# Performance work log

Hardware: AMD Instinct MI355X
Metric: run time of the kernel (lower is better)

Reference implementation:

```python
import jax, jax.numpy as jnp
import numpy as np

N = 50000      # nodes
E = 800000     # edges
D_IN = 300     # input node feature dim
D_H = 96       # hidden dim
D_OUT = 2      # classes
G = 64         # graphs in batch


def setup_inputs() -> dict:
    key = jax.random.key(0)
    ks = jax.random.split(key, 10)
    x = jax.random.normal(ks[0], (N, D_IN), dtype=jnp.float32)
    src = jax.random.randint(ks[1], (E,), 0, N, dtype=jnp.int32)
    dst = jax.random.randint(ks[2], (E,), 0, N, dtype=jnp.int32)
    batch = jnp.sort(jax.random.randint(ks[3], (N,), 0, G, dtype=jnp.int32))
    # GCNConv: linear weight (no bias in lin), separate additive bias (PyG default)
    W1 = jax.random.normal(ks[4], (D_IN, D_H), jnp.float32) / np.sqrt(D_IN)
    b1 = jnp.zeros((D_H,), jnp.float32)
    W2 = jax.random.normal(ks[5], (D_H, D_H), jnp.float32) / np.sqrt(D_H)
    b2 = jnp.zeros((D_H,), jnp.float32)
    Wfc = jax.random.normal(ks[6], (D_H, D_OUT), jnp.float32) / np.sqrt(D_H)
    bfc = jnp.zeros((D_OUT,), jnp.float32)
    return {"x": x, "W1": W1, "b1": b1, "W2": W2, "b2": b2,
            "Wfc": Wfc, "bfc": bfc, "src": src, "dst": dst, "batch": batch}


def _gcn_conv(h_in, W, b, src, dst, deg_inv_sqrt):
    """PyG GCNConv with self-loops: out = D^-1/2 (A+I) D^-1/2 (h W) + b."""
    h = h_in @ W                                   # [N, F] transform first
    norm = deg_inv_sqrt[src] * deg_inv_sqrt[dst]   # [E]
    msg = h[src] * norm[:, None]                   # gather + scale (dominant traffic)
    agg = jax.ops.segment_sum(msg, dst, num_segments=N)
    agg = agg + h * (deg_inv_sqrt * deg_inv_sqrt)[:, None]  # self-loop term
    return agg + b


def reference(x, W1, b1, W2, b2, Wfc, bfc, src, dst, batch):
    # degree with self loops, computed on destination nodes (PyG convention)
    deg = jax.ops.segment_sum(jnp.ones((E,), x.dtype), dst, num_segments=N) + 1.0
    dis = jax.lax.rsqrt(deg)
    h = jax.nn.relu(_gcn_conv(x, W1, b1, src, dst, dis))   # dropout = identity (eval)
    h = jax.nn.relu(_gcn_conv(h, W2, b2, src, dst, dis))
    # global mean pool over per-graph node segments
    counts = jax.ops.segment_sum(jnp.ones((N,), x.dtype), batch, num_segments=G)
    pooled = jax.ops.segment_sum(h, batch, num_segments=G) / jnp.maximum(counts, 1.0)[:, None]
    return pooled @ Wfc + bfc                               # [G, D_OUT]
```

## Files before the change

kernel.cpp:

```cpp
#include <hip/hip_runtime.h>
#include <hip/hip_bf16.h>

#define NN 50000
#define NE 800000
#define DIN 300
#define KP1 320
#define DH 96
#define DOUTC 2
#define NG 64

#define NKB 10
#define NFRAG (NKB * 6 * 64)

#define DSTRIDE 64
#define NB1 ((NN + 63) / 64)
#define EPB 1024
#define NB2 ((NN + 31) / 32)
#define LROW 104
#define QW 12

typedef __attribute__((ext_vector_type(8))) short bf16x8;
typedef __attribute__((ext_vector_type(4))) float f32x4;

__device__ inline unsigned short f2bf(float f) {
    unsigned int u = __float_as_uint(f);
    unsigned int r = (u + 0x7fffu + ((u >> 16) & 1u)) >> 16;
    return (unsigned short)r;
}
__device__ inline float b2f(unsigned short u) {
    return __uint_as_float((unsigned int)u << 16);
}
__device__ inline float blo(unsigned int u) { return __uint_as_float(u << 16); }
__device__ inline float bhi(unsigned int u) { return __uint_as_float(u & 0xffff0000u); }

__global__ void k_prep(int* cnt, float* pooled,
                       const float* __restrict__ W1, unsigned short* __restrict__ wt1f,
                       const float* __restrict__ W2, unsigned short* __restrict__ wt2) {
    int i = blockIdx.x * blockDim.x + threadIdx.x;
    if (i < NN) cnt[i] = 0;
    if (i < NG * DH) pooled[i] = 0.f;
    if (i < NFRAG * 8) {
        int j = i & 7;
        int f = i >> 3;
        int lane = f & 63;
        int ft = f >> 6;
        int t = ft % 6;
        int kb = ft / 6;
        int row = (lane & 15) + 16 * t;
        int col = kb * 32 + (lane >> 4) * 8 + j;
        wt1f[i] = (col < DIN) ? f2bf(W1[(size_t)col * DH + row]) : (unsigned short)0;
    }
    if (i < DH * DH) {
        int j = i / DH, k = i - j * DH;
        wt2[i] = f2bf(W2[(size_t)k * DH + j]);
    }
}

__global__ __launch_bounds__(256) void k_g1sc(const float* __restrict__ A,
        const unsigned short* __restrict__ WF, unsigned short* __restrict__ Cb,
        const int* __restrict__ src, const int* __restrict__ dst,
        int* cnt, unsigned short* __restrict__ esrc) {
    __shared__ unsigned short ldsB[NFRAG * 8];
    const int tid = threadIdx.x;

    if (blockIdx.x & 1) {
        const int ebase = (blockIdx.x >> 1) * EPB + tid * 4;
        if (ebase + 3 < NE) {
            int4 d4 = *(const int4*)&dst[ebase];
            int4 s4 = *(const int4*)&src[ebase];
            int p0 = atomicAdd(&cnt[d4.x], 1);
            int p1 = atomicAdd(&cnt[d4.y], 1);
            int p2 = atomicAdd(&cnt[d4.z], 1);
            int p3 = atomicAdd(&cnt[d4.w], 1);
            if (p0 < DSTRIDE) esrc[(size_t)d4.x * DSTRIDE + p0] = (unsigned short)s4.x;
            if (p1 < DSTRIDE) esrc[(size_t)d4.y * DSTRIDE + p1] = (unsigned short)s4.y;
            if (p2 < DSTRIDE) esrc[(size_t)d4.z * DSTRIDE + p2] = (unsigned short)s4.z;
            if (p3 < DSTRIDE) esrc[(size_t)d4.w * DSTRIDE + p3] = (unsigned short)s4.w;
        } else {
            for (int e = ebase; e < NE; ++e) {
                int d = dst[e];
                int pos = atomicAdd(&cnt[d], 1);
                if (pos < DSTRIDE) esrc[(size_t)d * DSTRIDE + pos] = (unsigned short)src[e];
            }
        }
        return;
    }

    const int tile = blockIdx.x >> 1;
    {
        const uint4* srcv = (const uint4*)WF;
        uint4* dstv = (uint4*)ldsB;
        #pragma unroll
        for (int f = 0; f < NFRAG / 256; ++f)
            dstv[f * 256 + tid] = srcv[f * 256 + tid];
    }
    __syncthreads();

    const int wv = tid >> 6;
    const int lane = tid & 63;
    const int m = lane & 15;
    const int quad = lane >> 4;
    const int row = tile * 64 + wv * 16 + m;
    const int arow = row < NN ? row : NN - 1;
    const float* ap = A + (size_t)arow * DIN + quad * 8;
    const float4 z4 = make_float4(0.f, 0.f, 0.f, 0.f);
    const bf16x8* lb = (const bf16x8*)ldsB;
    f32x4 acc[6];
    #pragma unroll
    for (int t = 0; t < 6; ++t) acc[t] = (f32x4){0.f, 0.f, 0.f, 0.f};

    float4 pa[4][2];
    #pragma unroll
    for (int i = 0; i < 3; ++i) {
        int kb = i * 32 + quad * 8;
        pa[i][0] = (kb + 4 <= DIN) ? *(const float4*)(ap + i * 32) : z4;
        pa[i][1] = (kb + 8 <= DIN) ? *(const float4*)(ap + i * 32 + 4) : z4;
    }

    #pragma unroll
    for (int i = 0; i < NKB; ++i) {
        if (i + 3 < NKB) {
            int kb = (i + 3) * 32 + quad * 8;
            pa[(i + 3) & 3][0] = (kb + 4 <= DIN) ? *(const float4*)(ap + (i + 3) * 32) : z4;
            pa[(i + 3) & 3][1] = (kb + 8 <= DIN) ? *(const float4*)(ap + (i + 3) * 32 + 4) : z4;
        }
        float4 a0 = pa[i & 3][0], a1 = pa[i & 3][1];
        bf16x8 af;
        af[0] = (short)f2bf(a0.x); af[1] = (short)f2bf(a0.y);
        af[2] = (short)f2bf(a0.z); af[3] = (short)f2bf(a0.w);
        af[4] = (short)f2bf(a1.x); af[5] = (short)f2bf(a1.y);
        af[6] = (short)f2bf(a1.z); af[7] = (short)f2bf(a1.w);
        #pragma unroll
        for (int t = 0; t < 6; ++t) {
            bf16x8 bf = lb[(i * 6 + t) * 64 + lane];
            acc[t] = __builtin_amdgcn_mfma_f32_16x16x32_bf16(af, bf, acc[t], 0, 0, 0);
        }
    }
    const int rbase = tile * 64 + wv * 16 + quad * 4;
    #pragma unroll
    for (int r = 0; r < 4; ++r) {
        int rr = rbase + r;
        if (rr < NN) {
            unsigned short* cp = Cb + (size_t)rr * DH + m;
            #pragma unroll
            for (int t = 0; t < 6; ++t) cp[t * 16] = f2bf(acc[t][r]);
        }
    }
}

__device__ inline void agg_row8(const uint4* __restrict__ hbq, const int* __restrict__ cnt,
                                const unsigned short* __restrict__ esrc,
                                int n, int q, float dn, int count, float* acc) {
    uint4 u0 = hbq[(size_t)n * QW + q];
    acc[0] = dn * blo(u0.x); acc[1] = dn * bhi(u0.x);
    acc[2] = dn * blo(u0.y); acc[3] = dn * bhi(u0.y);
    acc[4] = dn * blo(u0.z); acc[5] = dn * bhi(u0.z);
    acc[6] = dn * blo(u0.w); acc[7] = dn * bhi(u0.w);
    const int beg = n * DSTRIDE;
    const int end = beg + count;
    int e = beg;
    for (; e + 7 < end; e += 8) {
        int s0 = esrc[e],     s1 = esrc[e + 1], s2 = esrc[e + 2], s3 = esrc[e + 3];
        int s4 = esrc[e + 4], s5 = esrc[e + 5], s6 = esrc[e + 6], s7 = esrc[e + 7];
        uint4 v0 = hbq[(size_t)s0 * QW + q];
        uint4 v1 = hbq[(size_t)s1 * QW + q];
        uint4 v2 = hbq[(size_t)s2 * QW + q];
        uint4 v3 = hbq[(size_t)s3 * QW + q];
        uint4 v4 = hbq[(size_t)s4 * QW + q];
        uint4 v5 = hbq[(size_t)s5 * QW + q];
        uint4 v6 = hbq[(size_t)s6 * QW + q];
        uint4 v7 = hbq[(size_t)s7 * QW + q];
        float d0 = rsqrtf(1.0f + (float)cnt[s0]);
        float d1 = rsqrtf(1.0f + (float)cnt[s1]);
        float d2 = rsqrtf(1.0f + (float)cnt[s2]);
        float d3 = rsqrtf(1.0f + (float)cnt[s3]);
        float d4 = rsqrtf(1.0f + (float)cnt[s4]);
        float d5 = rsqrtf(1.0f + (float)cnt[s5]);
        float d6 = rsqrtf(1.0f + (float)cnt[s6]);
        float d7 = rsqrtf(1.0f + (float)cnt[s7]);
        acc[0] = fmaf(d0, blo(v0.x), acc[0]); acc[1] = fmaf(d0, bhi(v0.x), acc[1]);
        acc[2] = fmaf(d0, blo(v0.y), acc[2]); acc[3] = fmaf(d0, bhi(v0.y), acc[3]);
        acc[4] = fmaf(d0, blo(v0.z), acc[4]); acc[5] = fmaf(d0, bhi(v0.z), acc[5]);
        acc[6] = fmaf(d0, blo(v0.w), acc[6]); acc[7] = fmaf(d0, bhi(v0.w), acc[7]);
        acc[0] = fmaf(d1, blo(v1.x), acc[0]); acc[1] = fmaf(d1, bhi(v1.x), acc[1]);
        acc[2] = fmaf(d1, blo(v1.y), acc[2]); acc[3] = fmaf(d1, bhi(v1.y), acc[3]);
        acc[4] = fmaf(d1, blo(v1.z), acc[4]); acc[5] = fmaf(d1, bhi(v1.z), acc[5]);
        acc[6] = fmaf(d1, blo(v1.w), acc[6]); acc[7] = fmaf(d1, bhi(v1.w), acc[7]);
        acc[0] = fmaf(d2, blo(v2.x), acc[0]); acc[1] = fmaf(d2, bhi(v2.x), acc[1]);
        acc[2] = fmaf(d2, blo(v2.y), acc[2]); acc[3] = fmaf(d2, bhi(v2.y), acc[3]);
        acc[4] = fmaf(d2, blo(v2.z), acc[4]); acc[5] = fmaf(d2, bhi(v2.z), acc[5]);
        acc[6] = fmaf(d2, blo(v2.w), acc[6]); acc[7] = fmaf(d2, bhi(v2.w), acc[7]);
        acc[0] = fmaf(d3, blo(v3.x), acc[0]); acc[1] = fmaf(d3, bhi(v3.x), acc[1]);
        acc[2] = fmaf(d3, blo(v3.y), acc[2]); acc[3] = fmaf(d3, bhi(v3.y), acc[3]);
        acc[4] = fmaf(d3, blo(v3.z), acc[4]); acc[5] = fmaf(d3, bhi(v3.z), acc[5]);
        acc[6] = fmaf(d3, blo(v3.w), acc[6]); acc[7] = fmaf(d3, bhi(v3.w), acc[7]);
        acc[0] = fmaf(d4, blo(v4.x), acc[0]); acc[1] = fmaf(d4, bhi(v4.x), acc[1]);
        acc[2] = fmaf(d4, blo(v4.y), acc[2]); acc[3] = fmaf(d4, bhi(v4.y), acc[3]);
        acc[4] = fmaf(d4, blo(v4.z), acc[4]); acc[5] = fmaf(d4, bhi(v4.z), acc[5]);
        acc[6] = fmaf(d4, blo(v4.w), acc[6]); acc[7] = fmaf(d4, bhi(v4.w), acc[7]);
        acc[0] = fmaf(d5, blo(v5.x), acc[0]); acc[1] = fmaf(d5, bhi(v5.x), acc[1]);
        acc[2] = fmaf(d5, blo(v5.y), acc[2]); acc[3] = fmaf(d5, bhi(v5.y), acc[3]);
        acc[4] = fmaf(d5, blo(v5.z), acc[4]); acc[5] = fmaf(d5, bhi(v5.z), acc[5]);
        acc[6] = fmaf(d5, blo(v5.w), acc[6]); acc[7] = fmaf(d5, bhi(v5.w), acc[7]);
        acc[0] = fmaf(d6, blo(v6.x), acc[0]); acc[1] = fmaf(d6, bhi(v6.x), acc[1]);
        acc[2] = fmaf(d6, blo(v6.y), acc[2]); acc[3] = fmaf(d6, bhi(v6.y), acc[3]);
        acc[4] = fmaf(d6, blo(v6.z), acc[4]); acc[5] = fmaf(d6, bhi(v6.z), acc[5]);
        acc[6] = fmaf(d6, blo(v6.w), acc[6]); acc[7] = fmaf(d6, bhi(v6.w), acc[7]);
        acc[0] = fmaf(d7, blo(v7.x), acc[0]); acc[1] = fmaf(d7, bhi(v7.x), acc[1]);
        acc[2] = fmaf(d7, blo(v7.y), acc[2]); acc[3] = fmaf(d7, bhi(v7.y), acc[3]);
        acc[4] = fmaf(d7, blo(v7.z), acc[4]); acc[5] = fmaf(d7, bhi(v7.z), acc[5]);
        acc[6] = fmaf(d7, blo(v7.w), acc[6]); acc[7] = fmaf(d7, bhi(v7.w), acc[7]);
    }
    for (; e + 3 < end; e += 4) {
        int s0 = esrc[e], s1 = esrc[e + 1], s2 = esrc[e + 2], s3 = esrc[e + 3];
        float d0 = rsqrtf(1.0f + (float)cnt[s0]);
        float d1 = rsqrtf(1.0f + (float)cnt[s1]);
        float d2 = rsqrtf(1.0f + (float)cnt[s2]);
        float d3 = rsqrtf(1.0f + (float)cnt[s3]);
        uint4 v0 = hbq[(size_t)s0 * QW + q];
        uint4 v1 = hbq[(size_t)s1 * QW + q];
        uint4 v2 = hbq[(size_t)s2 * QW + q];
        uint4 v3 = hbq[(size_t)s3 * QW + q];
        acc[0] = fmaf(d0, blo(v0.x), acc[0]); acc[1] = fmaf(d0, bhi(v0.x), acc[1]);
        acc[2] = fmaf(d0, blo(v0.y), acc[2]); acc[3] = fmaf(d0, bhi(v0.y), acc[3]);
        acc[4] = fmaf(d0, blo(v0.z), acc[4]); acc[5] = fmaf(d0, bhi(v0.z), acc[5]);
        acc[6] = fmaf(d0, blo(v0.w), acc[6]); acc[7] = fmaf(d0, bhi(v0.w), acc[7]);
        acc[0] = fmaf(d1, blo(v1.x), acc[0]); acc[1] = fmaf(d1, bhi(v1.x), acc[1]);
        acc[2] = fmaf(d1, blo(v1.y), acc[2]); acc[3] = fmaf(d1, bhi(v1.y), acc[3]);
        acc[4] = fmaf(d1, blo(v1.z), acc[4]); acc[5] = fmaf(d1, bhi(v1.z), acc[5]);
        acc[6] = fmaf(d1, blo(v1.w), acc[6]); acc[7] = fmaf(d1, bhi(v1.w), acc[7]);
        acc[0] = fmaf(d2, blo(v2.x), acc[0]); acc[1] = fmaf(d2, bhi(v2.x), acc[1]);
        acc[2] = fmaf(d2, blo(v2.y), acc[2]); acc[3] = fmaf(d2, bhi(v2.y), acc[3]);
        acc[4] = fmaf(d2, blo(v2.z), acc[4]); acc[5] = fmaf(d2, bhi(v2.z), acc[5]);
        acc[6] = fmaf(d2, blo(v2.w), acc[6]); acc[7] = fmaf(d2, bhi(v2.w), acc[7]);
        acc[0] = fmaf(d3, blo(v3.x), acc[0]); acc[1] = fmaf(d3, bhi(v3.x), acc[1]);
        acc[2] = fmaf(d3, blo(v3.y), acc[2]); acc[3] = fmaf(d3, bhi(v3.y), acc[3]);
        acc[4] = fmaf(d3, blo(v3.z), acc[4]); acc[5] = fmaf(d3, bhi(v3.z), acc[5]);
        acc[6] = fmaf(d3, blo(v3.w), acc[6]); acc[7] = fmaf(d3, bhi(v3.w), acc[7]);
    }
    for (; e < end; ++e) {
        int s = esrc[e];
        float ds = rsqrtf(1.0f + (float)cnt[s]);
        uint4 v = hbq[(size_t)s * QW + q];
        acc[0] = fmaf(ds, blo(v.x), acc[0]); acc[1] = fmaf(ds, bhi(v.x), acc[1]);
        acc[2] = fmaf(ds, blo(v.y), acc[2]); acc[3] = fmaf(ds, bhi(v.y), acc[3]);
        acc[4] = fmaf(ds, blo(v.z), acc[4]); acc[5] = fmaf(ds, bhi(v.z), acc[5]);
        acc[6] = fmaf(ds, blo(v.w), acc[6]); acc[7] = fmaf(ds, bhi(v.w), acc[7]);
    }
}

__global__ __launch_bounds__(384) void k_agg1g2(const uint4* __restrict__ hbq,
        const int* __restrict__ cnt, const unsigned short* __restrict__ esrc,
        const float* __restrict__ b1, const unsigned short* __restrict__ WT,
        unsigned short* __restrict__ Cb) {
    __shared__ unsigned short a1l[32 * LROW];
    const int tid = threadIdx.x;
    const int n0 = blockIdx.x * 32;

    {
        int nl = tid / QW;
        int q = tid - nl * QW;
        int n = n0 + nl;
        uint4 o = make_uint4(0, 0, 0, 0);
        if (n < NN) {
            int count = cnt[n];
            float dn = rsqrtf(1.0f + (float)count);
            if (count > DSTRIDE) count = DSTRIDE;
            float acc[8];
            agg_row8(hbq, cnt, esrc, n, q, dn, count, acc);
            float r[8];
            #pragma unroll
            for (int k = 0; k < 8; ++k)
                r[k] = fmaxf(fmaf(dn, acc[k], b1[q * 8 + k]), 0.f);
            o.x = (unsigned int)f2bf(r[0]) | ((unsigned int)f2bf(r[1]) << 16);
            o.y = (unsigned int)f2bf(r[2]) | ((unsigned int)f2bf(r[3]) << 16);
            o.z = (unsigned int)f2bf(r[4]) | ((unsigned int)f2bf(r[5]) << 16);
            o.w = (unsigned int)f2bf(r[6]) | ((unsigned int)f2bf(r[7]) << 16);
        }
        *(uint4*)&a1l[nl * LROW + q * 8] = o;
    }
    __syncthreads();

    if (tid < 128) {
        const int wv = tid >> 6;
        const int lane = tid & 63;
        const int m = lane & 15;
        const int quad = lane >> 4;
        const unsigned short* ap = &a1l[(wv * 16 + m) * LROW + quad * 8];
        const unsigned short* wp = WT + (size_t)m * DH + quad * 8;
        bf16x8 af[3];
        #pragma unroll
        for (int i = 0; i < 3; ++i) af[i] = *(const bf16x8*)(ap + i * 32);
        const int rbase = n0 + wv * 16 + quad * 4;
        #pragma unroll 1
        for (int t = 0; t < 6; ++t) {
            f32x4 acc = (f32x4){0.f, 0.f, 0.f, 0.f};
            #pragma unroll
            for (int i = 0; i < 3; ++i) {
                bf16x8 bf = *(const bf16x8*)(wp + (size_t)t * 16 * DH + i * 32);
                acc = __builtin_amdgcn_mfma_f32_16x16x32_bf16(af[i], bf, acc, 0, 0, 0);
            }
            #pragma unroll
            for (int r = 0; r < 4; ++r) {
                int rr = rbase + r;
                if (rr < NN) Cb[(size_t)rr * DH + m + t * 16] = f2bf(acc[r]);
            }
        }
    }
}

__global__ __launch_bounds__(256) void k_agg2pool(const uint4* __restrict__ hbq,
        const int* __restrict__ cnt, const unsigned short* __restrict__ esrc,
        const float* __restrict__ b2, const int* __restrict__ batch,
        float* __restrict__ pooled) {
    __shared__ float lpool[4 * DH];
    __shared__ int g0s;
    const int tid = threadIdx.x;
    for (int i = tid; i < 4 * DH; i += 256) lpool[i] = 0.f;
    if (tid == 0) {
        int nfirst = (blockIdx.x * 256) / QW;
        g0s = batch[nfirst < NN ? nfirst : NN - 1];
    }
    __syncthreads();
    const int g0 = g0s;
    const int gid = blockIdx.x * 256 + tid;
    if (gid < NN * QW) {
        int n = gid / QW;
        int q = gid - n * QW;
        int count = cnt[n];
        float dn = rsqrtf(1.0f + (float)count);
        if (count > DSTRIDE) count = DSTRIDE;
        float acc[8];
        agg_row8(hbq, cnt, esrc, n, q, dn, count, acc);
        float r[8];
        #pragma unroll
        for (int k = 0; k < 8; ++k)
            r[k] = fmaxf(fmaf(dn, acc[k], b2[q * 8 + k]), 0.f);
        int g = batch[n];
        int slot = g - g0;
        if (slot < 4) {
            float* lp = &lpool[slot * DH + q * 8];
            #pragma unroll
            for (int k = 0; k < 8; ++k) atomicAdd(&lp[k], r[k]);
        } else {
            float* gp = &pooled[(size_t)g * DH + q * 8];
            #pragma unroll
            for (int k = 0; k < 8; ++k) atomicAdd(&gp[k], r[k]);
        }
    }
    __syncthreads();
    for (int i = tid; i < 4 * DH; i += 256) {
        float v = lpool[i];
        if (v != 0.f) {
            int slot = i / DH, f = i - slot * DH;
            atomicAdd(&pooled[(size_t)(g0 + slot) * DH + f], v);
        }
    }
}

__global__ void k_fc(const float* __restrict__ pooled, const int* __restrict__ batch,
                     const float* __restrict__ Wfc, const float* __restrict__ bfc,
                     float* __restrict__ out) {
    const int t = threadIdx.x;
    if (t >= NG * DOUTC) return;
    const int g = t / DOUTC;
    const int c = t - g * DOUTC;
    int lo = 0, hi = NN;
    while (lo < hi) { int mid = (lo + hi) >> 1; if (batch[mid] < g) lo = mid + 1; else hi = mid; }
    const int s = lo;
    hi = NN;
    while (lo < hi) { int mid = (lo + hi) >> 1; if (batch[mid] < g + 1) lo = mid + 1; else hi = mid; }
    float inv = 1.f / fmaxf((float)(lo - s), 1.f);
    float acc = bfc[c];
    #pragma unroll 8
    for (int j = 0; j < DH; ++j)
        acc += pooled[g * DH + j] * inv * Wfc[j * DOUTC + c];
    out[g * DOUTC + c] = acc;
}

extern "C" void kernel_launch(void* const* d_in, const int* in_sizes, int n_in,
                              void* d_out, int out_size, void* d_ws, size_t ws_size,
                              hipStream_t stream) {
    const float* x   = (const float*)d_in[0];
    const float* W1  = (const float*)d_in[1];
    const float* b1  = (const float*)d_in[2];
    const float* W2  = (const float*)d_in[3];
    const float* b2  = (const float*)d_in[4];
    const float* Wfc = (const float*)d_in[5];
    const float* bfc = (const float*)d_in[6];
    const int* src   = (const int*)d_in[7];
    const int* dst   = (const int*)d_in[8];
    const int* batch = (const int*)d_in[9];
    float* out = (float*)d_out;

    unsigned short* hb  = (unsigned short*)d_ws;
    unsigned short* h2b = hb + (size_t)NN * DH;
    float* pooled= (float*)(h2b + (size_t)NN * DH);
    int* cnt     = (int*)(pooled + NG * DH);
    unsigned short* esrc = (unsigned short*)(cnt + NN);
    unsigned short* wt1f = esrc + (size_t)NN * DSTRIDE;
    unsigned short* wt2  = wt1f + NFRAG * 8;

    const int TB = 256;
    k_prep<<<(NN + TB - 1) / TB, TB, 0, stream>>>(cnt, pooled, W1, wt1f, W2, wt2);
    k_g1sc<<<NB1 * 2, 256, 0, stream>>>(x, wt1f, hb, src, dst, cnt, esrc);
    k_agg1g2<<<NB2, 384, 0, stream>>>((const uint4*)hb, cnt, esrc, b1, wt2, h2b);
    k_agg2pool<<<(NN * QW + TB - 1) / TB, TB, 0, stream>>>(
        (const uint4*)h2b, cnt, esrc, b2, batch, pooled);
    k_fc<<<1, 128, 0, stream>>>(pooled, batch, Wfc, bfc, out);
}
```

Before: 250.7 us.

## Split each node's edge list across two thread halves in aggregation kernels

Both aggregation kernels now process 16 nodes per 384-thread block, and two threads share each (node, feature-quad) pair. Each thread gathers half of the node's edges, and the two partial sums are combined through shared memory. This doubles gather parallelism and memory-level parallelism per node, so each thread's serial edge chain is shorter and the long random-gather latency is better hidden. In exchange it adds an extra __syncthreads and shared-memory round trip, and the MFMA stage now uses only one wave per block.

```diff
diff --git a/kernel.cpp b/kernel.cpp
--- a/kernel.cpp
+++ b/kernel.cpp
@@ -15,7 +15,8 @@
 #define DSTRIDE 64
 #define NB1 ((NN + 63) / 64)
 #define EPB 1024
-#define NB2 ((NN + 31) / 32)
+#define NPB 16
+#define NBA ((NN + NPB - 1) / NPB)
 #define LROW 104
 #define QW 12
 
@@ -26,9 +27,6 @@
     unsigned int u = __float_as_uint(f);
     unsigned int r = (u + 0x7fffu + ((u >> 16) & 1u)) >> 16;
     return (unsigned short)r;
-}
-__device__ inline float b2f(unsigned short u) {
-    return __uint_as_float((unsigned int)u << 16);
 }
 __device__ inline float blo(unsigned int u) { return __uint_as_float(u << 16); }
 __device__ inline float bhi(unsigned int u) { return __uint_as_float(u & 0xffff0000u); }
@@ -148,17 +146,9 @@
     }
 }
 
-__device__ inline void agg_row8(const uint4* __restrict__ hbq, const int* __restrict__ cnt,
-                                const unsigned short* __restrict__ esrc,
-                                int n, int q, float dn, int count, float* acc) {
-    uint4 u0 = hbq[(size_t)n * QW + q];
-    acc[0] = dn * blo(u0.x); acc[1] = dn * bhi(u0.x);
-    acc[2] = dn * blo(u0.y); acc[3] = dn * bhi(u0.y);
-    acc[4] = dn * blo(u0.z); acc[5] = dn * bhi(u0.z);
-    acc[6] = dn * blo(u0.w); acc[7] = dn * bhi(u0.w);
-    const int beg = n * DSTRIDE;
-    const int end = beg + count;
-    int e = beg;
+__device__ inline void agg_edges(const uint4* __restrict__ hbq, const int* __restrict__ cnt,
+                                 const unsigned short* __restrict__ esrc,
+                                 int q, int e, int end, float* acc) {
     for (; e + 7 < end; e += 8) {
         int s0 = esrc[e],     s1 = esrc[e + 1], s2 = esrc[e + 2], s3 = esrc[e + 3];
         int s4 = esrc[e + 4], s5 = esrc[e + 5], s6 = esrc[e + 6], s7 = esrc[e + 7];
@@ -253,103 +243,156 @@
         const int* __restrict__ cnt, const unsigned short* __restrict__ esrc,
         const float* __restrict__ b1, const unsigned short* __restrict__ WT,
         unsigned short* __restrict__ Cb) {
-    __shared__ unsigned short a1l[32 * LROW];
+    __shared__ unsigned short a1l[NPB * LROW];
+    __shared__ float hacc[NPB * QW][8];
     const int tid = threadIdx.x;
-    const int n0 = blockIdx.x * 32;
-
-    {
-        int nl = tid / QW;
-        int q = tid - nl * QW;
-        int n = n0 + nl;
+    const int n0 = blockIdx.x * NPB;
+    const int h = tid / (NPB * QW);
+    const int r = tid - h * (NPB * QW);
+    const int nl = r / QW;
+    const int q = r - nl * QW;
+    const int n = n0 + nl;
+
+    int count = 0, beg = 0, c0 = 0;
+    float dn = 1.f;
+    if (n < NN) {
+        count = cnt[n];
+        dn = rsqrtf(1.0f + (float)count);
+        if (count > DSTRIDE) count = DSTRIDE;
+        beg = n * DSTRIDE;
+        c0 = count >> 1;
+    }
+    float acc[8] = {0.f, 0.f, 0.f, 0.f, 0.f, 0.f, 0.f, 0.f};
+    if (n < NN) {
+        if (h == 0) {
+            uint4 u0 = hbq[(size_t)n * QW + q];
+            acc[0] = dn * blo(u0.x); acc[1] = dn * bhi(u0.x);
+            acc[2] = dn * blo(u0.y); acc[3] = dn * bhi(u0.y);
+            acc[4] = dn * blo(u0.z); acc[5] = dn * bhi(u0.z);
+            acc[6] = dn * blo(u0.w); acc[7] = dn * bhi(u0.w);
+            agg_edges(hbq, cnt, esrc, q, beg, beg + c0, acc);
+        } else {
+            agg_edges(hbq, cnt, esrc, q, beg + c0, beg + count, acc);
+        }
+    }
+    if (h == 1) {
+        #pragma unroll
+        for (int k = 0; k < 8; ++k) hacc[r][k] = acc[k];
+    }
+    __syncthreads();
+    if (h == 0) {
         uint4 o = make_uint4(0, 0, 0, 0);
         if (n < NN) {
-            int count = cnt[n];
-            float dn = rsqrtf(1.0f + (float)count);
-            if (count > DSTRIDE) count = DSTRIDE;
-            float acc[8];
-            agg_row8(hbq, cnt, esrc, n, q, dn, count, acc);
-            float r[8];
+            const float* hp = hacc[r];
+            float rr[8];
             #pragma unroll
             for (int k = 0; k < 8; ++k)
-                r[k] = fmaxf(fmaf(dn, acc[k], b1[q * 8 + k]), 0.f);
-            o.x = (unsigned int)f2bf(r[0]) | ((unsigned int)f2bf(r[1]) << 16);
-            o.y = (unsigned int)f2bf(r[2]) | ((unsigned int)f2bf(r[3]) << 16);
-            o.z = (unsigned int)f2bf(r[4]) | ((unsigned int)f2bf(r[5]) << 16);
-            o.w = (unsigned int)f2bf(r[6]) | ((unsigned int)f2bf(r[7]) << 16);
+                rr[k] = fmaxf(fmaf(dn, acc[k] + hp[k], b1[q * 8 + k]), 0.f);
+            o.x = (unsigned int)f2bf(rr[0]) | ((unsigned int)f2bf(rr[1]) << 16);
+            o.y = (unsigned int)f2bf(rr[2]) | ((unsigned int)f2bf(rr[3]) << 16);
+            o.z = (unsigned int)f2bf(rr[4]) | ((unsigned int)f2bf(rr[5]) << 16);
+            o.w = (unsigned int)f2bf(rr[6]) | ((unsigned int)f2bf(rr[7]) << 16);
         }
         *(uint4*)&a1l[nl * LROW + q * 8] = o;
     }
     __syncthreads();
 
-    if (tid < 128) {
-        const int wv = tid >> 6;
-        const int lane = tid & 63;
+    if (tid < 64) {
+        const int lane = tid;
         const int m = lane & 15;
         const int quad = lane >> 4;
-        const unsigned short* ap = &a1l[(wv * 16 + m) * LROW + quad * 8];
+        const unsigned short* ap = &a1l[m * LROW + quad * 8];
         const unsigned short* wp = WT + (size_t)m * DH + quad * 8;
         bf16x8 af[3];
         #pragma unroll
         for (int i = 0; i < 3; ++i) af[i] = *(const bf16x8*)(ap + i * 32);
-        const int rbase = n0 + wv * 16 + quad * 4;
+        const int rbase = n0 + quad * 4;
         #pragma unroll 1
         for (int t = 0; t < 6; ++t) {
-            f32x4 acc = (f32x4){0.f, 0.f, 0.f, 0.f};
+            f32x4 acc2 = (f32x4){0.f, 0.f, 0.f, 0.f};
             #pragma unroll
             for (int i = 0; i < 3; ++i) {
                 bf16x8 bf = *(const bf16x8*)(wp + (size_t)t * 16 * DH + i * 32);
-                acc = __builtin_amdgcn_mfma_f32_16x16x32_bf16(af[i], bf, acc, 0, 0, 0);
+                acc2 = __builtin_amdgcn_mfma_f32_16x16x32_bf16(af[i], bf, acc2, 0, 0, 0);
             }
             #pragma unroll
-            for (int r = 0; r < 4; ++r) {
-                int rr = rbase + r;
-                if (rr < NN) Cb[(size_t)rr * DH + m + t * 16] = f2bf(acc[r]);
+            for (int rr2 = 0; rr2 < 4; ++rr2) {
+                int row = rbase + rr2;
+                if (row < NN) Cb[(size_t)row * DH + m + t * 16] = f2bf(acc2[rr2]);
             }
         }
     }
 }
 
-__global__ __launch_bounds__(256) void k_agg2pool(const uint4* __restrict__ hbq,
+__global__ __launch_bounds__(384) void k_agg2pool(const uint4* __restrict__ hbq,
         const int* __restrict__ cnt, const unsigned short* __restrict__ esrc,
         const float* __restrict__ b2, const int* __restrict__ batch,
         float* __restrict__ pooled) {
     __shared__ float lpool[4 * DH];
+    __shared__ float hacc[NPB * QW][8];
     __shared__ int g0s;
     const int tid = threadIdx.x;
-    for (int i = tid; i < 4 * DH; i += 256) lpool[i] = 0.f;
+    for (int i = tid; i < 4 * DH; i += 384) lpool[i] = 0.f;
     if (tid == 0) {
-        int nfirst = (blockIdx.x * 256) / QW;
-        g0s = batch[nfirst < NN ? nfirst : NN - 1];
+        int nf = blockIdx.x * NPB;
+        g0s = batch[nf < NN ? nf : NN - 1];
     }
     __syncthreads();
     const int g0 = g0s;
-    const int gid = blockIdx.x * 256 + tid;
-    if (gid < NN * QW) {
-        int n = gid / QW;
-        int q = gid - n * QW;
-        int count = cnt[n];
-        float dn = rsqrtf(1.0f + (float)count);
+    const int n0 = blockIdx.x * NPB;
+    const int h = tid / (NPB * QW);
+    const int r = tid - h * (NPB * QW);
+    const int nl = r / QW;
+    const int q = r - nl * QW;
+    const int n = n0 + nl;
+
+    int count = 0, beg = 0, c0 = 0;
+    float dn = 1.f;
+    if (n < NN) {
+        count = cnt[n];
+        dn = rsqrtf(1.0f + (float)count);
         if (count > DSTRIDE) count = DSTRIDE;
-        float acc[8];
-        agg_row8(hbq, cnt, esrc, n, q, dn, count, acc);
-        float r[8];
+        beg = n * DSTRIDE;
+        c0 = count >> 1;
+    }
+    float acc[8] = {0.f, 0.f, 0.f, 0.f, 0.f, 0.f, 0.f, 0.f};
+    if (n < NN) {
+        if (h == 0) {
+            uint4 u0 = hbq[(size_t)n * QW + q];
+            acc[0] = dn * blo(u0.x); acc[1] = dn * bhi(u0.x);
+            acc[2] = dn * blo(u0.y); acc[3] = dn * bhi(u0.y);
+            acc[4] = dn * blo(u0.z); acc[5] = dn * bhi(u0.z);
+            acc[6] = dn * blo(u0.w); acc[7] = dn * bhi(u0.w);
+            agg_edges(hbq, cnt, esrc, q, beg, beg + c0, acc);
+        } else {
+            agg_edges(hbq, cnt, esrc, q, beg + c0, beg + count, acc);
+        }
+    }
+    if (h == 1) {
+        #pragma unroll
+        for (int k = 0; k < 8; ++k) hacc[r][k] = acc[k];
+    }
+    __syncthreads();
+    if (h == 0 && n < NN) {
+        const float* hp = hacc[r];
+        float rr[8];
         #pragma unroll
         for (int k = 0; k < 8; ++k)
-            r[k] = fmaxf(fmaf(dn, acc[k], b2[q * 8 + k]), 0.f);
+            rr[k] = fmaxf(fmaf(dn, acc[k] + hp[k], b2[q * 8 + k]), 0.f);
         int g = batch[n];
         int slot = g - g0;
         if (slot < 4) {
             float* lp = &lpool[slot * DH + q * 8];
             #pragma unroll
-            for (int k = 0; k < 8; ++k) atomicAdd(&lp[k], r[k]);
+            for (int k = 0; k < 8; ++k) atomicAdd(&lp[k], rr[k]);
         } else {
             float* gp = &pooled[(size_t)g * DH + q * 8];
             #pragma unroll
-            for (int k = 0; k < 8; ++k) atomicAdd(&gp[k], r[k]);
-        }
-    }
-    __syncthreads();
-    for (int i = tid; i < 4 * DH; i += 256) {
+            for (int k = 0; k < 8; ++k) atomicAdd(&gp[k], rr[k]);
+        }
+    }
+    __syncthreads();
+    for (int i = tid; i < 4 * DH; i += 384) {
         float v = lpool[i];
         if (v != 0.f) {
             int slot = i / DH, f = i - slot * DH;
@@ -404,8 +447,8 @@
     const int TB = 256;
     k_prep<<<(NN + TB - 1) / TB, TB, 0, stream>>>(cnt, pooled, W1, wt1f, W2, wt2);
     k_g1sc<<<NB1 * 2, 256, 0, stream>>>(x, wt1f, hb, src, dst, cnt, esrc);
-    k_agg1g2<<<NB2, 384, 0, stream>>>((const uint4*)hb, cnt, esrc, b1, wt2, h2b);
-    k_agg2pool<<<(NN * QW + TB - 1) / TB, TB, 0, stream>>>(
+    k_agg1g2<<<NBA, 384, 0, stream>>>((const uint4*)hb, cnt, esrc, b1, wt2, h2b);
+    k_agg2pool<<<NBA, 384, 0, stream>>>(
         (const uint4*)h2b, cnt, esrc, b2, batch, pooled);
     k_fc<<<1, 128, 0, stream>>>(pooled, batch, Wfc, bfc, out);
 }
```

After: 282.6 us. +12.8%, slower.
